# Kernel optimization log

Measured on AMD Instinct MI355X. Metric: run time of the kernel, lower is better.

Reference implementation:

```python
import jax, jax.numpy as jnp
import numpy as np

DIM = 512
NUM_HEADS = 8
HEAD_DIM = DIM // NUM_HEADS
B, S = 2, 2048


def setup_inputs() -> dict:
    key = jax.random.key(0)
    ks = jax.random.split(key, 16)
    scale = 1.0 / np.sqrt(DIM)
    inp = {
        "x": jax.random.normal(ks[0], (B, S, DIM), dtype=jnp.float32),
        "Qexpl": jax.random.normal(ks[1], (B, S, DIM), dtype=jnp.float32),
        "Kexpl": jax.random.normal(ks[2], (B, S, DIM), dtype=jnp.float32),
        "fl": jax.random.uniform(ks[3], (B,), dtype=jnp.float32),
        "fu": jax.random.uniform(ks[4], (B,), dtype=jnp.float32),
        "age": jax.random.uniform(ks[5], (B,), dtype=jnp.float32),
        "gender": jax.random.uniform(ks[6], (B,), dtype=jnp.float32),
        # Linear params: weight stored as [out, in] like torch; y = x @ W.T + b
        "Wq": jax.random.normal(ks[7], (DIM, DIM), dtype=jnp.float32) * scale,
        "bq": jnp.zeros((DIM,), dtype=jnp.float32),
        "Wk": jax.random.normal(ks[8], (DIM, DIM), dtype=jnp.float32) * scale,
        "bk": jnp.zeros((DIM,), dtype=jnp.float32),
        "Wv": jax.random.normal(ks[9], (DIM, DIM), dtype=jnp.float32) * scale,
        "bv": jnp.zeros((DIM,), dtype=jnp.float32),
        "Wo": jax.random.normal(ks[10], (DIM, DIM), dtype=jnp.float32) * scale,
        "bo": jnp.zeros((DIM,), dtype=jnp.float32),
    }
    return inp


def reference(x, Qexpl, Kexpl, fl, fu, age, gender, Wq, bq, Wk, bk, Wv, bv, Wo, bo):
    # drofe_fn is None -> Q/K projections used directly.
    Q = Qexpl @ Wq.T + bq            # [B, S, D]
    K = Kexpl @ Wk.T + bk            # [B, S, D]
    V = x @ Wv.T + bv                # [B, S, D]

    def split_heads(t):  # [B, S, D] -> [B, H, S, hd]
        return t.reshape(B, S, NUM_HEADS, HEAD_DIM).transpose(0, 2, 1, 3)

    Qh, Kh, Vh = split_heads(Q), split_heads(K), split_heads(V)
    scale = 1.0 / np.sqrt(HEAD_DIM).astype(np.float32)
    scores = jnp.einsum("bhqd,bhkd->bhqk", Qh, Kh) * scale  # [B, H, S, S]
    weights = jax.nn.softmax(scores, axis=-1)
    attn = jnp.einsum("bhqk,bhkd->bhqd", weights, Vh)        # [B, H, S, hd]
    attn = attn.transpose(0, 2, 1, 3).reshape(B, S, DIM)
    return attn @ Wo.T + bo
```

## Files before the change

### kernel.cpp

```cpp
#include <hip/hip_runtime.h>
#include <hip/hip_bf16.h>

typedef unsigned short ushort_t;
typedef __attribute__((ext_vector_type(8))) short bf16x8;
typedef __attribute__((ext_vector_type(4))) float f32x4;

__device__ __forceinline__ ushort_t f2bf(float f) {
    union { float f; unsigned u; } v; v.f = f;
    unsigned r = v.u + 0x7FFF + ((v.u >> 16) & 1);
    return (ushort_t)(r >> 16);
}
__device__ __forceinline__ float bfl(ushort_t u) {
    union { unsigned u; float f; } v; v.u = (unsigned)u << 16; return v.f;
}
__device__ __forceinline__ bf16x8 ld8(const ushort_t* p) { return *(const bf16x8*)p; }

__device__ __forceinline__ unsigned cvt2(float x, float y) {
    __hip_bfloat162 h = __float22bfloat162_rn(make_float2(x, y));
    unsigned r; __builtin_memcpy(&r, &h, 4); return r;
}
__device__ __forceinline__ bf16x8 pack8f(float4 a, float4 b) {
    union { unsigned u[4]; bf16x8 v; } o;
    o.u[0] = cvt2(a.x, a.y); o.u[1] = cvt2(a.z, a.w);
    o.u[2] = cvt2(b.x, b.y); o.u[3] = cvt2(b.z, b.w);
    return o.v;
}

__device__ __forceinline__ void gload_lds16(const ushort_t* g, ushort_t* l) {
    __builtin_amdgcn_global_load_lds(
        (const __attribute__((address_space(1))) void*)g,
        (__attribute__((address_space(3))) void*)l, 16, 0, 0);
}

__global__ __launch_bounds__(256)
void cast_kernel(const float* __restrict__ Qe, const float* __restrict__ Ke,
                 const float* __restrict__ x,  const float* __restrict__ Wq,
                 const float* __restrict__ Wk, const float* __restrict__ Wv,
                 const float* __restrict__ Wo,
                 ushort_t* __restrict__ Ab, ushort_t* __restrict__ Wb)
{
    const unsigned i8 = (blockIdx.x * 256u + threadIdx.x) * 8u;
    const float* src; ushort_t* dst;
    if (i8 < (3u << 21)) {
        unsigned a = i8 >> 21, off = i8 & ((1u << 21) - 1);
        src = (a == 0 ? Qe : a == 1 ? Ke : x) + off;
        dst = Ab + i8;
    } else {
        unsigned j = i8 - (3u << 21);
        unsigned a = j >> 18, off = j & ((1u << 18) - 1);
        src = (a == 0 ? Wq : a == 1 ? Wk : a == 2 ? Wv : Wo) + off;
        dst = Wb + j;
    }
    *(bf16x8*)dst = pack8f(*(const float4*)src, *(const float4*)(src + 4));
}

__global__ __launch_bounds__(256, 3)
void proj_qkv_kernel(const ushort_t* __restrict__ Ab, const ushort_t* __restrict__ Wb,
                     const float* __restrict__ bq, const float* __restrict__ bk,
                     const float* __restrict__ bv,
                     ushort_t* __restrict__ Qo, ushort_t* __restrict__ Ko,
                     ushort_t* __restrict__ Vt)
{
    __shared__ ushort_t smem[2 * 12288];

    const int z = blockIdx.z;
    const ushort_t* A = Ab + ((size_t)z << 21);
    const ushort_t* W = Wb + ((size_t)z << 18);
    const float* bias = (z == 0) ? bq : (z == 1) ? bk : bv;

    const int m0 = blockIdx.y * 64, n0 = blockIdx.x * 128;
    const int t = threadIdx.x;
    const int lane = t & 63, wave = t >> 6;
    const int wm = (wave & 1) * 32, wn = (wave >> 1) * 64;
    const int fr = lane & 15, quad = lane >> 4;
    const int fr7 = fr & 7;

    const int arl = wave * 16 + (lane >> 3);
    const ushort_t* ag = A + (size_t)(m0 + arl) * 512 + (((lane & 7) ^ (arl & 7)) << 3);
    const int dbA = wave * 16 * 64;
    const int wrl = wave * 32 + (lane >> 3);
    const ushort_t* wg = W + (size_t)(n0 + wrl) * 512 + (((lane & 7) ^ (wrl & 7)) << 3);
    const int dbW = 4096 + wave * 32 * 64;

    f32x4 acc[2][4] = {};

#pragma unroll
    for (int i = 0; i < 2; ++i)
        gload_lds16(ag + (size_t)(i * 8) * 512, smem + dbA + i * 512);
#pragma unroll
    for (int i = 0; i < 4; ++i)
        gload_lds16(wg + (size_t)(i * 8) * 512, smem + dbW + i * 512);
    __syncthreads();

    for (int kk = 0; kk < 8; ++kk) {
        ushort_t* cur = smem + (kk & 1) * 12288;
        ushort_t* nxt = smem + ((kk & 1) ^ 1) * 12288;
        if (kk < 7) {
            int ko = (kk + 1) * 64;
#pragma unroll
            for (int i = 0; i < 2; ++i)
                gload_lds16(ag + ko + (size_t)(i * 8) * 512, nxt + dbA + i * 512);
#pragma unroll
            for (int i = 0; i < 4; ++i)
                gload_lds16(wg + ko + (size_t)(i * 8) * 512, nxt + dbW + i * 512);
        }

#pragma unroll
        for (int ks = 0; ks < 2; ++ks) {
            bf16x8 af[2], bfr[4];
#pragma unroll
            for (int mt = 0; mt < 2; ++mt)
                af[mt] = ld8(cur + (wm + mt * 16 + fr) * 64 + (((ks * 4 + quad) ^ fr7) << 3));
#pragma unroll
            for (int nt = 0; nt < 4; ++nt)
                bfr[nt] = ld8(cur + 4096 + (wn + nt * 16 + fr) * 64 + (((ks * 4 + quad) ^ fr7) << 3));
#pragma unroll
            for (int mt = 0; mt < 2; ++mt)
#pragma unroll
                for (int nt = 0; nt < 4; ++nt)
                    acc[mt][nt] = __builtin_amdgcn_mfma_f32_16x16x32_bf16(
                        af[mt], bfr[nt], acc[mt][nt], 0, 0, 0);
        }
        asm volatile("s_waitcnt vmcnt(0)" ::: "memory");
        __builtin_amdgcn_s_barrier();
        __builtin_amdgcn_sched_barrier(0);
    }

    const float C1 = 0.125f * 1.44269504088896340736f;
    if (z != 2) {
        ushort_t* dst = (z == 0) ? Qo : Ko;
#pragma unroll
        for (int nt = 0; nt < 4; ++nt) {
            int n = n0 + wn + nt * 16 + fr;
            float bb = bias[n];
#pragma unroll
            for (int mt = 0; mt < 2; ++mt) {
                int mb = m0 + wm + mt * 16 + quad * 4;
                if (z == 0) {
#pragma unroll
                    for (int r = 0; r < 4; ++r)
                        dst[(size_t)(mb + r) * 512 + n] = f2bf((acc[mt][nt][r] + bb) * C1);
                } else {
#pragma unroll
                    for (int r = 0; r < 4; ++r)
                        dst[(size_t)(mb + r) * 512 + n] = f2bf(acc[mt][nt][r] + bb);
                }
            }
        }
    } else {
        ushort_t* lT = smem;
#pragma unroll
        for (int nt = 0; nt < 4; ++nt) {
            int nl = wn + nt * 16 + fr;
            float bb = bias[n0 + nl];
#pragma unroll
            for (int mt = 0; mt < 2; ++mt) {
                int tm = wm + mt * 16 + quad * 4;
#pragma unroll
                for (int r = 0; r < 4; ++r) {
                    int tl = tm + r;
                    int sg = (tl & 32) + ((tl & 12) << 1) + ((tl >> 4 & 1) << 2) + (tl & 3);
                    lT[nl * 72 + sg] = f2bf(acc[mt][nt][r] + bb);
                }
            }
        }
        __syncthreads();
        const int bidx = m0 >> 11, m0t = m0 & 2047;
#pragma unroll
        for (int i = 0; i < 4; ++i) {
            int s = i * 256 + t;
            int row = s >> 3, c = s & 7;
            int n = n0 + row;
            int h = n >> 6, d = n & 63;
            bf16x8 v = ld8(lT + row * 72 + c * 8);
            *(bf16x8*)(Vt + ((size_t)((bidx * 8 + h) * 64 + d)) * 2048 + m0t + c * 8) = v;
        }
    }
}

__global__ __launch_bounds__(256, 2)
void gemm_o_kernel(const ushort_t* __restrict__ Oh, const float* __restrict__ Lsum,
                   const ushort_t* __restrict__ W, const float* __restrict__ bias,
                   float* __restrict__ dst)
{
    __shared__ ushort_t lA[64 * 72];
    __shared__ ushort_t lB[64 * 72];
    const int m0 = blockIdx.y * 64, n0 = blockIdx.x * 64;
    const int t = threadIdx.x;
    const int lane = t & 63, wave = t >> 6;
    const int wm = (wave & 1) * 32, wn = (wave >> 1) * 32;
    const int fr = lane & 15, quad = lane >> 4;
    const int bq_ = m0 >> 11, qq0 = m0 & 2047;

    f32x4 acc[2][2] = {};
    bf16x8 va0[2], va1[2], vw[2];
    float l0[2], l1[2];

#pragma unroll
    for (int i = 0; i < 2; ++i) {
        int s = i * 256 + t;
        int r = s >> 3, jp = s & 7;
        va0[i] = ld8(Oh + (size_t)(m0 + r) * 512 + jp * 8);
        va1[i] = ld8(Oh + (size_t)(m0 + r + 4096) * 512 + jp * 8);
        l0[i] = Lsum[(bq_ * 8 + 0) * 2048 + qq0 + r];
        l1[i] = Lsum[((2 + bq_) * 8 + 0) * 2048 + qq0 + r];
        vw[i] = ld8(W + (size_t)(n0 + r) * 512 + jp * 8);
    }

    for (int kk = 0; kk < 8; ++kk) {
        if (kk) __syncthreads();
#pragma unroll
        for (int i = 0; i < 2; ++i) {
            int s = i * 256 + t;
            int r = s >> 3, jp = s & 7;
            float inv = 1.f / (l0[i] + l1[i]);
            union { bf16x8 v; ushort_t s8[8]; } a0, a1;
            a0.v = va0[i]; a1.v = va1[i];
            union { unsigned u[4]; bf16x8 v; } o;
#pragma unroll
            for (int j = 0; j < 4; ++j)
                o.u[j] = cvt2((bfl(a0.s8[2 * j]) + bfl(a1.s8[2 * j])) * inv,
                              (bfl(a0.s8[2 * j + 1]) + bfl(a1.s8[2 * j + 1])) * inv);
            *(bf16x8*)(lA + r * 72 + jp * 8) = o.v;
            *(bf16x8*)(lB + r * 72 + jp * 8) = vw[i];
        }
        __syncthreads();
        if (kk < 7) {
            int k0 = (kk + 1) * 64;
#pragma unroll
            for (int i = 0; i < 2; ++i) {
                int s = i * 256 + t;
                int r = s >> 3, jp = s & 7;
                va0[i] = ld8(Oh + (size_t)(m0 + r) * 512 + k0 + jp * 8);
                va1[i] = ld8(Oh + (size_t)(m0 + r + 4096) * 512 + k0 + jp * 8);
                l0[i] = Lsum[(bq_ * 8 + kk + 1) * 2048 + qq0 + r];
                l1[i] = Lsum[((2 + bq_) * 8 + kk + 1) * 2048 + qq0 + r];
                vw[i] = ld8(W + (size_t)(n0 + r) * 512 + k0 + jp * 8);
            }
        }

        bf16x8 af[2][2], bfrag[2][2];
#pragma unroll
        for (int ks = 0; ks < 2; ++ks) {
#pragma unroll
            for (int mt = 0; mt < 2; ++mt)
                af[mt][ks] = ld8(lA + (wm + mt * 16 + fr) * 72 + (ks * 4 + quad) * 8);
#pragma unroll
            for (int nt = 0; nt < 2; ++nt)
                bfrag[nt][ks] = ld8(lB + (wn + nt * 16 + fr) * 72 + (ks * 4 + quad) * 8);
        }
#pragma unroll
        for (int ks = 0; ks < 2; ++ks)
#pragma unroll
            for (int mt = 0; mt < 2; ++mt)
#pragma unroll
                for (int nt = 0; nt < 2; ++nt)
                    acc[mt][nt] = __builtin_amdgcn_mfma_f32_16x16x32_bf16(
                        af[mt][ks], bfrag[nt][ks], acc[mt][nt], 0, 0, 0);
    }

#pragma unroll
    for (int nt = 0; nt < 2; ++nt) {
        int n = n0 + wn + nt * 16 + fr;
        float bb = bias[n];
#pragma unroll
        for (int mt = 0; mt < 2; ++mt) {
            int mb = m0 + wm + mt * 16 + quad * 4;
#pragma unroll
            for (int r = 0; r < 4; ++r)
                dst[(size_t)(mb + r) * 512 + n] = acc[mt][nt][r] + bb;
        }
    }
}

__global__ __launch_bounds__(256, 4)
void attn_kernel(const ushort_t* __restrict__ Q, const ushort_t* __restrict__ K,
                 const ushort_t* __restrict__ Vt, ushort_t* __restrict__ Opart,
                 float* __restrict__ Lsum)
{
    __shared__ ushort_t lK[128 * 64];
    __shared__ ushort_t lV[64 * 128];

    const int b = blockIdx.z >> 1, half = blockIdx.z & 1;
    const int h = blockIdx.y;
    const int q0 = blockIdx.x * 64;
    const int kvbase = half * 1024;
    const int t = threadIdx.x;
    const int lane = t & 63, w = t >> 6;
    const int wq = w * 16;
    const int fr = lane & 15, quad = lane >> 4;
    const int fr7 = fr & 7;

    bf16x8 aq[2];
    {
        const ushort_t* qp = Q + (size_t)(b * 2048 + q0 + wq + fr) * 512 + h * 64 + quad * 8;
        aq[0] = ld8(qp);
        aq[1] = ld8(qp + 32);
    }

    const int krl = w * 32 + (lane >> 3);
    const ushort_t* kg = K + (size_t)(b * 2048 + kvbase + krl) * 512 + h * 64
                           + (lane & 7) * 8;
    ushort_t* lk_wr = lK + krl * 64 + (((lane & 7) ^ (krl & 7)) << 3);

    const int vrl = w * 4 + (lane >> 4);
    const ushort_t* vbase = Vt + (size_t)((b * 8 + h) * 64 + vrl) * 2048 + kvbase
                              + (((lane & 15) ^ (vrl & 7)) << 3);

    const ushort_t* kr0 = lK + fr * 64 + ((quad ^ fr7) << 3);
    const ushort_t* kr1 = lK + fr * 64 + (((4 + quad) ^ fr7) << 3);
    const ushort_t* vr0 = lV + fr * 128 + (((0 * 4 + quad) ^ fr7) << 3);
    const ushort_t* vr1 = lV + fr * 128 + (((1 * 4 + quad) ^ fr7) << 3);
    const ushort_t* vr2 = lV + fr * 128 + (((2 * 4 + quad) ^ fr7) << 3);
    const ushort_t* vr3 = lV + fr * 128 + (((3 * 4 + quad) ^ fr7) << 3);
    const ushort_t* vr[4] = { vr0, vr1, vr2, vr3 };

    bf16x8 kreg[4];
#pragma unroll
    for (int i = 0; i < 4; ++i)
        kreg[i] = ld8(kg + (size_t)(i * 8) * 512);
#pragma unroll
    for (int i = 0; i < 4; ++i)
        *(bf16x8*)(lk_wr + i * 8 * 64) = kreg[i];
    __syncthreads();

    f32x4 oacc[4] = {};
    float lsum = 0.f;

    for (int tt = 0; tt < 8; ++tt) {
        const int kv = tt << 7;

#pragma unroll
        for (int i = 0; i < 4; ++i)
            gload_lds16(vbase + kv + (size_t)(i * 16) * 2048, lV + (i * 16 + w * 4) * 128);
        __builtin_amdgcn_sched_barrier(0);
        if (tt < 7) {
#pragma unroll
            for (int i = 0; i < 4; ++i)
                kreg[i] = ld8(kg + (size_t)(kv + 128 + i * 8) * 512);
        }
        __builtin_amdgcn_sched_barrier(0);

        f32x4 sc[8] = {};
        __builtin_amdgcn_s_setprio(1);
#pragma unroll
        for (int nt = 0; nt < 8; ++nt) {
            bf16x8 kb = ld8(kr0 + nt * 16 * 64);
            sc[nt] = __builtin_amdgcn_mfma_f32_16x16x32_bf16(kb, aq[0], sc[nt], 0, 0, 0);
        }
#pragma unroll
        for (int nt = 0; nt < 8; ++nt) {
            bf16x8 kb = ld8(kr1 + nt * 16 * 64);
            sc[nt] = __builtin_amdgcn_mfma_f32_16x16x32_bf16(kb, aq[1], sc[nt], 0, 0, 0);
        }
        __builtin_amdgcn_s_setprio(0);

        if (tt < 7) asm volatile("s_waitcnt vmcnt(4)" ::: "memory");
        else        asm volatile("s_waitcnt vmcnt(0)" ::: "memory");
        __builtin_amdgcn_s_barrier();
        __builtin_amdgcn_sched_barrier(0);

        __builtin_amdgcn_s_setprio(1);
#pragma unroll
        for (int ks = 0; ks < 4; ++ks) {
            float p0[4], p1[4];
#pragma unroll
            for (int r = 0; r < 4; ++r) p0[r] = exp2f(sc[2 * ks][r]);
#pragma unroll
            for (int r = 0; r < 4; ++r) p1[r] = exp2f(sc[2 * ks + 1][r]);
            lsum += ((p0[0] + p0[1]) + (p0[2] + p0[3]))
                  + ((p1[0] + p1[1]) + (p1[2] + p1[3]));
            union { unsigned u[4]; bf16x8 v; } pa;
            pa.u[0] = cvt2(p0[0], p0[1]); pa.u[1] = cvt2(p0[2], p0[3]);
            pa.u[2] = cvt2(p1[0], p1[1]); pa.u[3] = cvt2(p1[2], p1[3]);
#pragma unroll
            for (int nt = 0; nt < 4; ++nt) {
                bf16x8 vb = ld8(vr[ks] + nt * 16 * 128);
                oacc[nt] = __builtin_amdgcn_mfma_f32_16x16x32_bf16(pa.v, vb, oacc[nt], 0, 0, 0);
            }
            if (ks == 0 && tt < 7) {
#pragma unroll
                for (int i = 0; i < 4; ++i)
                    *(bf16x8*)(lk_wr + i * 8 * 64) = kreg[i];
            }
        }
        __builtin_amdgcn_s_setprio(0);
        __syncthreads();
    }

    float rs = lsum;
    rs += __shfl_xor(rs, 16, 64);
    rs += __shfl_xor(rs, 32, 64);
#pragma unroll
    for (int r = 0; r < 4; ++r) {
        int qrow = q0 + wq + quad * 4 + r;
        ushort_t* od = Opart + ((size_t)(half * 2 + b) * 2048 + qrow) * 512 + h * 64;
#pragma unroll
        for (int nt = 0; nt < 4; ++nt)
            od[nt * 16 + fr] = f2bf(oacc[nt][r]);
    }
    if (lane < 16)
        Lsum[((half * 2 + b) * 8 + h) * 2048 + q0 + wq + lane] = rs;
}

extern "C" void kernel_launch(void* const* d_in, const int* in_sizes, int n_in,
                              void* d_out, int out_size, void* d_ws, size_t ws_size,
                              hipStream_t stream) {
    const float* x   = (const float*)d_in[0];
    const float* Qe  = (const float*)d_in[1];
    const float* Ke  = (const float*)d_in[2];
    const float* Wq  = (const float*)d_in[7];
    const float* bq  = (const float*)d_in[8];
    const float* Wk  = (const float*)d_in[9];
    const float* bk  = (const float*)d_in[10];
    const float* Wv  = (const float*)d_in[11];
    const float* bv  = (const float*)d_in[12];
    const float* Wo  = (const float*)d_in[13];
    const float* bo  = (const float*)d_in[14];

    const size_t NTOK = 2 * 2048;
    const size_t ACT = NTOK * 512;

    ushort_t* p = (ushort_t*)d_ws;
    ushort_t* Abf = p; p += (size_t)3 << 21;
    ushort_t* Wbf = p; p += (size_t)4 << 18;
    ushort_t* Qws = p; p += ACT;
    ushort_t* Kws = p; p += ACT;
    ushort_t* Vt  = p; p += ACT;
    ushort_t* OpH = p; p += 2 * ACT;
    float* Lsum  = (float*)p;

    cast_kernel<<<dim3(3584), 256, 0, stream>>>(Qe, Ke, x, Wq, Wk, Wv, Wo, Abf, Wbf);
    proj_qkv_kernel<<<dim3(4, 64, 3), 256, 0, stream>>>(Abf, Wbf, bq, bk, bv,
                                                        Qws, Kws, Vt);
    attn_kernel<<<dim3(32, 8, 4), 256, 0, stream>>>(Qws, Kws, Vt, OpH, Lsum);
    gemm_o_kernel<<<dim3(8, 64), 256, 0, stream>>>(OpH, Lsum, Wbf + ((size_t)3 << 18),
                                                   bo, (float*)d_out);
}
```

Before: 154.6 us.

## Fuse activation fp32-to-bf16 cast into QKV projection GEMM loads

Removes the separate cast pass over the three fp32 activation tensors. The projection kernel now loads fp32 rows into registers, converts them to bf16 and writes them into swizzled LDS, while the weights stay on the async global-to-LDS path. This drops a full read-write round trip of the activations through a bf16 workspace. In exchange, the A loads become synchronous register loads, so there is less overlap, and each tile is reloaded by the 4 N-blocks in fp32, which is twice the bytes of bf16.

```diff
diff --git a/kernel.cpp b/kernel.cpp
--- a/kernel.cpp
+++ b/kernel.cpp
@@ -33,29 +33,19 @@
 }
 
 __global__ __launch_bounds__(256)
-void cast_kernel(const float* __restrict__ Qe, const float* __restrict__ Ke,
-                 const float* __restrict__ x,  const float* __restrict__ Wq,
-                 const float* __restrict__ Wk, const float* __restrict__ Wv,
-                 const float* __restrict__ Wo,
-                 ushort_t* __restrict__ Ab, ushort_t* __restrict__ Wb)
+void cast_w_kernel(const float* __restrict__ Wq, const float* __restrict__ Wk,
+                   const float* __restrict__ Wv, const float* __restrict__ Wo,
+                   ushort_t* __restrict__ Wb)
 {
     const unsigned i8 = (blockIdx.x * 256u + threadIdx.x) * 8u;
-    const float* src; ushort_t* dst;
-    if (i8 < (3u << 21)) {
-        unsigned a = i8 >> 21, off = i8 & ((1u << 21) - 1);
-        src = (a == 0 ? Qe : a == 1 ? Ke : x) + off;
-        dst = Ab + i8;
-    } else {
-        unsigned j = i8 - (3u << 21);
-        unsigned a = j >> 18, off = j & ((1u << 18) - 1);
-        src = (a == 0 ? Wq : a == 1 ? Wk : a == 2 ? Wv : Wo) + off;
-        dst = Wb + j;
-    }
-    *(bf16x8*)dst = pack8f(*(const float4*)src, *(const float4*)(src + 4));
+    unsigned a = i8 >> 18, off = i8 & ((1u << 18) - 1);
+    const float* src = (a == 0 ? Wq : a == 1 ? Wk : a == 2 ? Wv : Wo) + off;
+    *(bf16x8*)(Wb + i8) = pack8f(*(const float4*)src, *(const float4*)(src + 4));
 }
 
 __global__ __launch_bounds__(256, 3)
-void proj_qkv_kernel(const ushort_t* __restrict__ Ab, const ushort_t* __restrict__ Wb,
+void proj_qkv_kernel(const float* __restrict__ Qe, const float* __restrict__ Ke,
+                     const float* __restrict__ x,  const ushort_t* __restrict__ Wb,
                      const float* __restrict__ bq, const float* __restrict__ bk,
                      const float* __restrict__ bv,
                      ushort_t* __restrict__ Qo, ushort_t* __restrict__ Ko,
@@ -64,7 +54,7 @@
     __shared__ ushort_t smem[2 * 12288];
 
     const int z = blockIdx.z;
-    const ushort_t* A = Ab + ((size_t)z << 21);
+    const float* Af = (z == 0) ? Qe : (z == 1) ? Ke : x;
     const ushort_t* W = Wb + ((size_t)z << 18);
     const float* bias = (z == 0) ? bq : (z == 1) ? bk : bv;
 
@@ -75,21 +65,27 @@
     const int fr = lane & 15, quad = lane >> 4;
     const int fr7 = fr & 7;
 
-    const int arl = wave * 16 + (lane >> 3);
-    const ushort_t* ag = A + (size_t)(m0 + arl) * 512 + (((lane & 7) ^ (arl & 7)) << 3);
-    const int dbA = wave * 16 * 64;
+    const int ar = t >> 2;
+    const float* ags = Af + (size_t)(m0 + ar) * 512 + (t & 3) * 16;
+    const int c0 = (t & 3) * 2;
+    const int awo0 = ar * 64 + (((c0    ) ^ (ar & 7)) << 3);
+    const int awo1 = ar * 64 + (((c0 + 1) ^ (ar & 7)) << 3);
+
     const int wrl = wave * 32 + (lane >> 3);
     const ushort_t* wg = W + (size_t)(n0 + wrl) * 512 + (((lane & 7) ^ (wrl & 7)) << 3);
     const int dbW = 4096 + wave * 32 * 64;
 
     f32x4 acc[2][4] = {};
-
-#pragma unroll
-    for (int i = 0; i < 2; ++i)
-        gload_lds16(ag + (size_t)(i * 8) * 512, smem + dbA + i * 512);
+    float4 fa[4];
+
+#pragma unroll
+    for (int j = 0; j < 4; ++j) fa[j] = *(const float4*)(ags + j * 4);
 #pragma unroll
     for (int i = 0; i < 4; ++i)
         gload_lds16(wg + (size_t)(i * 8) * 512, smem + dbW + i * 512);
+    asm volatile("s_waitcnt vmcnt(0)" ::: "memory");
+    *(bf16x8*)(smem + awo0) = pack8f(fa[0], fa[1]);
+    *(bf16x8*)(smem + awo1) = pack8f(fa[2], fa[3]);
     __syncthreads();
 
     for (int kk = 0; kk < 8; ++kk) {
@@ -98,8 +94,7 @@
         if (kk < 7) {
             int ko = (kk + 1) * 64;
 #pragma unroll
-            for (int i = 0; i < 2; ++i)
-                gload_lds16(ag + ko + (size_t)(i * 8) * 512, nxt + dbA + i * 512);
+            for (int j = 0; j < 4; ++j) fa[j] = *(const float4*)(ags + ko + j * 4);
 #pragma unroll
             for (int i = 0; i < 4; ++i)
                 gload_lds16(wg + ko + (size_t)(i * 8) * 512, nxt + dbW + i * 512);
@@ -122,6 +117,11 @@
                         af[mt], bfr[nt], acc[mt][nt], 0, 0, 0);
         }
         asm volatile("s_waitcnt vmcnt(0)" ::: "memory");
+        if (kk < 7) {
+            *(bf16x8*)(nxt + awo0) = pack8f(fa[0], fa[1]);
+            *(bf16x8*)(nxt + awo1) = pack8f(fa[2], fa[3]);
+        }
+        asm volatile("s_waitcnt lgkmcnt(0)" ::: "memory");
         __builtin_amdgcn_s_barrier();
         __builtin_amdgcn_sched_barrier(0);
     }
@@ -422,7 +422,6 @@
     const size_t ACT = NTOK * 512;
 
     ushort_t* p = (ushort_t*)d_ws;
-    ushort_t* Abf = p; p += (size_t)3 << 21;
     ushort_t* Wbf = p; p += (size_t)4 << 18;
     ushort_t* Qws = p; p += ACT;
     ushort_t* Kws = p; p += ACT;
@@ -430,8 +429,8 @@
     ushort_t* OpH = p; p += 2 * ACT;
     float* Lsum  = (float*)p;
 
-    cast_kernel<<<dim3(3584), 256, 0, stream>>>(Qe, Ke, x, Wq, Wk, Wv, Wo, Abf, Wbf);
-    proj_qkv_kernel<<<dim3(4, 64, 3), 256, 0, stream>>>(Abf, Wbf, bq, bk, bv,
+    cast_w_kernel<<<dim3(512), 256, 0, stream>>>(Wq, Wk, Wv, Wo, Wbf);
+    proj_qkv_kernel<<<dim3(4, 64, 3), 256, 0, stream>>>(Qe, Ke, x, Wbf, bq, bk, bv,
                                                         Qws, Kws, Vt);
     attn_kernel<<<dim3(32, 8, 4), 256, 0, stream>>>(Qws, Kws, Vt, OpH, Lsum);
     gemm_o_kernel<<<dim3(8, 64), 256, 0, stream>>>(OpH, Lsum, Wbf + ((size_t)3 << 18),
```

Measured after the change: 159.7 us. 3.3% more time.
